# Performance work log

Measured on AMD Instinct MI355X. Metric: run time of the kernel, lower is better.

Reference implementation:

```python
import jax, jax.numpy as jnp
from jax import lax
import numpy as np

B, PEP, MHC, V, H, C, K, NH, FLAT = 1024, 15, 44, 21, 9, 3200, 9, 800, 21 * 59
EPS = 1e-5


def setup_inputs() -> dict:
    key = jax.random.key(0)
    ks = jax.random.split(key, 24)
    n = lambda k, s: jax.random.normal(k, s, dtype=jnp.float32) * 0.05
    inp = {
        'pep': jax.random.normal(ks[0], (B, PEP, V), dtype=jnp.float32),
        'mhc': jax.random.normal(ks[1], (B, MHC, V), dtype=jnp.float32),
        # conv module (bias=True inside CapHLA_EL)
        'W1': n(ks[2], (2 * C, V)), 'b1': n(ks[3], (2 * C,)),
        'Wd': n(ks[4], (C, 1, K)), 'bd': n(ks[5], (C,)),
        'bn1_g': jnp.ones((C,), jnp.float32), 'bn1_b': jnp.zeros((C,), jnp.float32),
        'bn1_m': jnp.zeros((C,), jnp.float32), 'bn1_v': jnp.ones((C,), jnp.float32),
        'W2': n(ks[6], (V, C)), 'b2': n(ks[7], (V,)),
        # shared LayerNorm(vocab_size)
        'ln_g': jnp.ones((V,), jnp.float32), 'ln_b': jnp.zeros((V,), jnp.float32),
        # MHA (bias=False)
        'Wq': n(ks[8], (V, V * H)), 'Wk': n(ks[9], (V, V * H)),
        'Wv': n(ks[10], (V, V * H)), 'Wo': n(ks[11], (V * H, V)),
        # feature selection head
        'Wf1': n(ks[12], (FLAT, NH)), 'bf1': n(ks[13], (NH,)),
        'bn2_g': jnp.ones((NH,), jnp.float32), 'bn2_b': jnp.zeros((NH,), jnp.float32),
        'bn2_m': jnp.zeros((NH,), jnp.float32), 'bn2_v': jnp.ones((NH,), jnp.float32),
        'Wf2': n(ks[14], (NH, 64)), 'bf2': n(ks[15], (64,)),
        'Wf3': n(ks[16], (64, 2)), 'bf3': n(ks[17], (2,)),
    }
    return inp


def _ln(x, g, b):
    m = x.mean(-1, keepdims=True)
    v = x.var(-1, keepdims=True)
    return (x - m) * lax.rsqrt(v + EPS) * g + b


def _forward(pep, mhc, W1, b1, Wd, bd, bn1_g, bn1_b, bn1_m, bn1_v, W2, b2,
             ln_g, ln_b, Wq, Wk, Wv, Wo,
             Wf1, bf1, bn2_g, bn2_b, bn2_m, bn2_v, Wf2, bf2, Wf3, bf3):
    X = jnp.concatenate([pep, mhc], axis=1)  # [B, 59, V]
    residual = X
    # ---- convolution module (channels-first) ----
    x = X.transpose(0, 2, 1)                               # [B, V, L]
    x = jnp.einsum('bcl,oc->bol', x, W1) + b1[None, :, None]   # [B, 2C, L]
    a, g = jnp.split(x, 2, axis=1)
    x = a * jax.nn.sigmoid(g)                              # GLU -> [B, C, L]
    x = lax.conv_general_dilated(x, Wd, window_strides=(1,), padding=[((K - 1) // 2, (K - 1) // 2)],
                                 dimension_numbers=('NCH', 'OIH', 'NCH'),
                                 feature_group_count=C) + bd[None, :, None]
    x = (x - bn1_m[None, :, None]) * lax.rsqrt(bn1_v + EPS)[None, :, None] * bn1_g[None, :, None] + bn1_b[None, :, None]
    x = jax.nn.silu(x)
    x = jnp.einsum('bcl,oc->bol', x, W2) + b2[None, :, None]  # [B, V, L]
    X = _ln(residual + x.transpose(0, 2, 1), ln_g, ln_b)
    residual = X
    # ---- multi-head self-attention (head_dim == V) ----
    Bn, S, D = X.shape
    def heads(W):
        return (X @ W).reshape(Bn, S, H, D).transpose(0, 2, 1, 3)  # [B, H, S, D]
    q, k, v = heads(Wq), heads(Wk), heads(Wv)
    scores = jnp.einsum('bhqd,bhkd->bhqk', q, k) / jnp.sqrt(jnp.float32(D))
    attn = jax.nn.softmax(scores, axis=-1)
    o = jnp.einsum('bhqk,bhkd->bhqd', attn, v)
    o = o.transpose(0, 2, 1, 3).reshape(Bn, S, H * D) @ Wo
    X = _ln(residual + o, ln_g, ln_b)
    # ---- feature selection head ----
    h = X.reshape(Bn, -1) @ Wf1 + bf1
    h = jax.nn.silu(h)
    h = (h - bn2_m) * lax.rsqrt(bn2_v + EPS) * bn2_g + bn2_b
    h = jax.nn.relu(h @ Wf2 + bf2)
    return h @ Wf3 + bf3                                   # [B, 2]


def reference(pep, mhc, W1, b1, Wd, bd, bn1_g, bn1_b, bn1_m, bn1_v, W2, b2,
              ln_g, ln_b, Wq, Wk, Wv, Wo,
              Wf1, bf1, bn2_g, bn2_b, bn2_m, bn2_v, Wf2, bf2, Wf3, bf3):
    return _forward(pep, mhc, W1, b1, Wd, bd, bn1_g, bn1_b, bn1_m, bn1_v, W2, b2,
                    ln_g, ln_b, Wq, Wk, Wv, Wo,
                    Wf1, bf1, bn2_g, bn2_b, bn2_m, bn2_v, Wf2, bf2, Wf3, bf3)
```

## Files before the change

kernel.cpp:

```cpp
#include <hip/hip_runtime.h>
#include <hip/hip_bf16.h>

namespace {

constexpr int B   = 1024;
constexpr int PEP = 15;
constexpr int MHCN = 44;
constexpr int S   = 59;
constexpr int V   = 21;
constexpr int C   = 3200;
constexpr int KW  = 9;
constexpr int H   = 9;
constexpr int NH  = 800;
constexpr int SV  = S * V;
constexpr int HD  = H * V;
constexpr int XF  = 1248;
constexpr float EPSF = 1e-5f;
constexpr int CHALF = 25;
constexpr float NLOG2E = -1.4426950408889634f;

typedef __attribute__((ext_vector_type(8))) short short8;
typedef __attribute__((ext_vector_type(4))) float f32x4;
typedef __attribute__((ext_vector_type(2))) float f32x2;

__device__ __forceinline__ float sigm(float x) {
  return __builtin_amdgcn_rcpf(1.f + __expf(-x));
}
__device__ __forceinline__ unsigned short f2bf(float f) {
  unsigned r;
  asm("v_cvt_pk_bf16_f32 %0, %1, %2" : "=v"(r) : "v"(f), "v"(f));
  return (unsigned short)r;
}
__device__ __forceinline__ unsigned pkbf(float a, float b) {
  unsigned r;
  asm("v_cvt_pk_bf16_f32 %0, %1, %2" : "=v"(r) : "v"(a), "v"(b));
  return r;
}
__device__ __forceinline__ float bflo(unsigned d) {
  union { unsigned u; float f; } v; v.u = d << 16; return v.f;
}
__device__ __forceinline__ float bfhi(unsigned d) {
  union { unsigned u; float f; } v; v.u = d & 0xffff0000u; return v.f;
}

__global__ void k_packW(const float* __restrict__ W1, const float* __restrict__ b1,
                        const float* __restrict__ Wd,
                        const float* __restrict__ bd, const float* __restrict__ g,
                        const float* __restrict__ bb, const float* __restrict__ m,
                        const float* __restrict__ vv, const float* __restrict__ W2,
                        const float* __restrict__ Wq, const float* __restrict__ Wk,
                        const float* __restrict__ Wv, const float* __restrict__ Wo,
                        const float* __restrict__ Wf1,
                        unsigned short* __restrict__ FB1, unsigned short* __restrict__ FB2,
                        unsigned short* __restrict__ FQKV, unsigned short* __restrict__ FWo,
                        unsigned short* __restrict__ FWf1, float* __restrict__ TAP) {
  int id = blockIdx.x * 256 + threadIdx.x;
  if (id < 400 * 64) {
    int tau = id >> 6, l = id & 63;
    int ci = tau >> 3, tt = tau & 7;
    int lr = l & 15, lg = l >> 4;
    bool isg = (tt >= 4);
    int row = (!isg) ? (ci * 64 + tt * 16 + lr) : (C + ci * 64 + (tt - 4) * 16 + lr);
    float sc = isg ? NLOG2E : 1.f;
    for (int j = 0; j < 8; ++j) {
      int k = lg * 8 + j;
      float val = (k < V) ? W1[row * V + k] * sc : (k == V ? b1[row] * sc : 0.f);
      FB1[(size_t)tau * 512 + l * 8 + j] = f2bf(val);
    }
  } else if (id < 38400) {
    int id2 = id - 25600;
    int sg = id2 >> 6, l = id2 & 63;
    int ci = sg >> 2, rem = sg & 3, kt = rem >> 1, nt = rem & 1;
    int lr = l & 15, lg = l >> 4;
    int vc = nt * 16 + lr;
    for (int j = 0; j < 8; ++j) {
      int ch = ci * 64 + kt * 32 + lg * 8 + j;
      float val = (vc < V) ? W2[(size_t)vc * C + ch] : 0.f;
      FB2[(size_t)sg * 512 + l * 8 + j] = f2bf(val);
    }
  } else if (id < 41856) {
    int id2 = id - 38400;
    int tile = id2 >> 6, l = id2 & 63;
    int h = tile / 6, rem = tile - h * 6;
    int mat = rem >> 1, nt = rem & 1;
    int lr = l & 15, kg = l >> 4;
    int dcol = nt * 16 + lr;
    const float* W = (mat == 0) ? Wq : (mat == 1) ? Wk : Wv;
    const float scale = (mat == 0) ? 0.21821789023599236f : 1.f;
    for (int j = 0; j < 8; ++j) {
      int u = kg * 8 + j;
      float val = (u < V && dcol < V) ? W[u * HD + h * V + dcol] * scale : 0.f;
      FQKV[(size_t)tile * 512 + l * 8 + j] = f2bf(val);
    }
  } else if (id < 43008) {
    int id2 = id - 41856;
    int tile = id2 >> 6, l = id2 & 63;
    int h = tile >> 1, nt = tile & 1;
    int lr = l & 15, kg = l >> 4;
    int vcol = nt * 16 + lr;
    for (int j = 0; j < 8; ++j) {
      int d = kg * 8 + j;
      float val = (d < V && vcol < V) ? Wo[(h * V + d) * V + vcol] : 0.f;
      FWo[(size_t)tile * 512 + l * 8 + j] = f2bf(val);
    }
  } else if (id < 46208) {
    int c = id - 43008;
    if (c < C) {
      float sc = g[c] * rsqrtf(vv[c] + EPSF);
      for (int k = 0; k < KW; ++k) TAP[c * 12 + k] = Wd[c * KW + k] * sc;
      TAP[c * 12 + 9]  = (bd[c] - m[c]) * sc + bb[c];
      TAP[c * 12 + 10] = 0.f;
      TAP[c * 12 + 11] = 0.f;
    }
  } else if (id < 46208 + 1950 * 64) {
    int id2 = id - 46208;
    int tile = id2 >> 6, l = id2 & 63;
    int ntg = tile / 39, kk = tile - ntg * 39;
    int lr = l & 15, kg = l >> 4;
    int n = ntg * 16 + lr;
    for (int j = 0; j < 8; ++j) {
      int f = kk * 32 + kg * 8 + j;
      float val = (f < SV) ? Wf1[(size_t)f * NH + n] : 0.f;
      FWf1[(size_t)tile * 512 + l * 8 + j] = f2bf(val);
    }
  }
}

constexpr int GST = 74;

__device__ __forceinline__ void glu_chunk(const unsigned short* fb1p, unsigned* glw0,
                                          short8 ax, int mt, int mypos) {
  f32x4 ga[4], gg[4];
#pragma unroll
  for (int tt = 0; tt < 4; ++tt) {
    short8 bf = *reinterpret_cast<const short8*>(fb1p + tt * 512);
    ga[tt] = __builtin_amdgcn_mfma_f32_16x16x32_bf16(ax, bf, (f32x4){0.f, 0.f, 0.f, 0.f}, 0, 0, 0);
  }
#pragma unroll
  for (int tt = 0; tt < 4; ++tt) {
    short8 bf = *reinterpret_cast<const short8*>(fb1p + (4 + tt) * 512);
    gg[tt] = __builtin_amdgcn_mfma_f32_16x16x32_bf16(ax, bf, (f32x4){0.f, 0.f, 0.f, 0.f}, 0, 0, 0);
  }
  if (mt < 3) {
#pragma unroll
    for (int tt = 0; tt < 4; ++tt) {
      unsigned* gw = glw0 + tt * (16 * GST / 2);
      float s0 = __builtin_amdgcn_rcpf(1.f + __builtin_amdgcn_exp2f(gg[tt][0]));
      float s1 = __builtin_amdgcn_rcpf(1.f + __builtin_amdgcn_exp2f(gg[tt][1]));
      float s2 = __builtin_amdgcn_rcpf(1.f + __builtin_amdgcn_exp2f(gg[tt][2]));
      float s3 = __builtin_amdgcn_rcpf(1.f + __builtin_amdgcn_exp2f(gg[tt][3]));
      gw[0] = pkbf(ga[tt][0] * s0, ga[tt][1] * s1);
      gw[1] = pkbf(ga[tt][2] * s2, ga[tt][3] * s3);
    }
  } else {
#pragma unroll
    for (int tt = 0; tt < 4; ++tt) {
      unsigned* gw = glw0 + tt * (16 * GST / 2);
      float g0 = (mypos + 0 < S) ? ga[tt][0] * __builtin_amdgcn_rcpf(1.f + __builtin_amdgcn_exp2f(gg[tt][0])) : 0.f;
      float g1 = (mypos + 1 < S) ? ga[tt][1] * __builtin_amdgcn_rcpf(1.f + __builtin_amdgcn_exp2f(gg[tt][1])) : 0.f;
      float g2 = (mypos + 2 < S) ? ga[tt][2] * __builtin_amdgcn_rcpf(1.f + __builtin_amdgcn_exp2f(gg[tt][2])) : 0.f;
      float g3 = (mypos + 3 < S) ? ga[tt][3] * __builtin_amdgcn_rcpf(1.f + __builtin_amdgcn_exp2f(gg[tt][3])) : 0.f;
      gw[0] = pkbf(g0, g1);
      gw[1] = pkbf(g2, g3);
    }
  }
}

__device__ __forceinline__ void conv_chunk(const unsigned* glr, const float* tapp,
                                           const unsigned short* fb2p,
                                           unsigned short* sbw, const unsigned short* sbr,
                                           int mt, f32x4 (&acc2)[2]) {
  const float4 t0 = *reinterpret_cast<const float4*>(tapp);
  const float4 t1 = *reinterpret_cast<const float4*>(tapp + 4);
  const float4 t2 = *reinterpret_cast<const float4*>(tapp + 8);
  const float tap[9] = {t0.x, t0.y, t0.z, t0.w, t1.x, t1.y, t1.z, t1.w, t2.x};
  const float sh = t2.y;
  float gv[24];
#pragma unroll
  for (int i2 = 0; i2 < 12; ++i2) {
    const unsigned d = glr[i2];
    gv[2 * i2]     = bflo(d);
    gv[2 * i2 + 1] = bfhi(d);
  }
  f32x2 q[16];
#pragma unroll
  for (int j = 0; j < 16; ++j) q[j] = (f32x2){gv[j], gv[j + 8]};
#pragma unroll
  for (int i2 = 0; i2 < 8; ++i2) {
    f32x2 ac = (f32x2){sh, sh};
#pragma unroll
    for (int k = 0; k < KW; ++k) {
      f32x2 tk = (f32x2){tap[k], tap[k]};
      ac = ac + q[i2 + k] * tk;
    }
    const float a0 = ac.x, a1 = ac.y;
    const float s0 = a0 * __builtin_amdgcn_rcpf(1.f + __builtin_amdgcn_exp2f(a0 * NLOG2E));
    const float s1 = a1 * __builtin_amdgcn_rcpf(1.f + __builtin_amdgcn_exp2f(a1 * NLOG2E));
    sbw[i2 * 72] = f2bf(s0);
    unsigned short hv = f2bf(s1);
    if (mt == 3 && i2 >= 3) hv = 0;
    sbw[(i2 + 8) * 72] = hv;
  }
#pragma unroll
  for (int kt = 0; kt < 2; ++kt) {
    short8 a2f = *reinterpret_cast<const short8*>(sbr + kt * 32);
#pragma unroll
    for (int nt = 0; nt < 2; ++nt) {
      short8 b2f = *reinterpret_cast<const short8*>(fb2p + (kt * 2 + nt) * 512);
      acc2[nt] = __builtin_amdgcn_mfma_f32_16x16x32_bf16(a2f, b2f, acc2[nt], 0, 0, 0);
    }
  }
}

__global__ __launch_bounds__(512) void k_conv(
    const float* __restrict__ pep, const float* __restrict__ mhc,
    const unsigned short* __restrict__ FB1, const unsigned short* __restrict__ FB2,
    const float* __restrict__ TAP, float* __restrict__ Yp) {
  __shared__ __align__(16) unsigned char smem[2 * 64 * GST * 2 + 4 * 16 * 72 * 2];
  unsigned short* Xbf = reinterpret_cast<unsigned short*>(smem);
  unsigned short* glA = reinterpret_cast<unsigned short*>(smem);
  unsigned short* glB = glA + 64 * GST;
  unsigned short* Sb  = glB + 64 * GST;
  const int t = threadIdx.x;
  const int b = blockIdx.x >> 1;
  const int half = blockIdx.x & 1;
  const int lane = t & 63;
  const int w = t >> 6;
  const int lr = lane & 15;
  const int lg = lane >> 4;
  const bool isGlu = (w < 4);
  const int mt = isGlu ? w : (w - 4);
  const int mypos = mt * 16 + lg * 4;

  if (t < 256) {
    const int row = t >> 2, q = t & 3;
    const float* xr = (row < PEP) ? pep + ((size_t)b * PEP + row) * V
                    : (row < S)   ? mhc + ((size_t)b * MHCN + (row - PEP)) * V
                                  : nullptr;
#pragma unroll
    for (int i2 = 0; i2 < 5; ++i2) {
      int c0 = q * 10 + 2 * i2;
      float f0 = (xr && c0 < V) ? xr[c0] : 0.f;
      float f1 = (xr && c0 + 1 < V) ? xr[c0 + 1] : ((xr && c0 + 1 == V) ? 1.f : 0.f);
      *reinterpret_cast<unsigned*>(&Xbf[row * 40 + c0]) = pkbf(f0, f1);
    }
  }
  __syncthreads();

  short8 ax = {};
  if (isGlu) ax = *reinterpret_cast<const short8*>(&Xbf[(mt * 16 + lr) * 40 + lg * 8]);
  __syncthreads();

  if (t < 256) {
    unsigned short* buf = (t < 128) ? glA : glB;
    const int i2 = t & 127;
    *reinterpret_cast<unsigned*>(&buf[(i2 >> 1) * GST + (i2 & 1) * 2]) = 0u;
  }

  f32x4 acc2[2];
  acc2[0] = (f32x4){0.f, 0.f, 0.f, 0.f};
  acc2[1] = (f32x4){0.f, 0.f, 0.f, 0.f};

  unsigned* glwA = reinterpret_cast<unsigned*>(&glA[lr * GST + 4 + mypos]);
  unsigned* glwB = reinterpret_cast<unsigned*>(&glB[lr * GST + 4 + mypos]);
  const unsigned* glrA = reinterpret_cast<const unsigned*>(&glA[lane * GST + mt * 16]);
  const unsigned* glrB = reinterpret_cast<const unsigned*>(&glB[lane * GST + mt * 16]);
  unsigned short* sbw = Sb + mt * (16 * 72) + lane;
  const unsigned short* sbr = Sb + mt * (16 * 72) + lr * 72 + lg * 8;
  const unsigned short* fb1p = FB1 + (size_t)half * CHALF * 8 * 512 + lane * 8;
  const unsigned short* fb2p = FB2 + (size_t)half * CHALF * 4 * 512 + lane * 8;
  const float* tapp = TAP + ((size_t)half * CHALF * 64 + lane) * 12;

  if (isGlu) glu_chunk(fb1p, glwA, ax, mt, mypos);
  __syncthreads();

  for (int p = 0; p < 12; ++p) {
    if (isGlu) glu_chunk(fb1p + 4096, glwB, ax, mt, mypos);
    else       conv_chunk(glrA, tapp, fb2p, sbw, sbr, mt, acc2);
    __syncthreads();
    if (isGlu) glu_chunk(fb1p + 2 * 4096, glwA, ax, mt, mypos);
    else       conv_chunk(glrB, tapp + 768, fb2p + 2048, sbw, sbr, mt, acc2);
    __syncthreads();
    fb1p += 2 * 4096;
    fb2p += 2 * 2048;
    tapp += 2 * 768;
  }
  if (!isGlu) {
    conv_chunk(glrA, tapp, fb2p, sbw, sbr, mt, acc2);
    float* yp = Yp + (size_t)blockIdx.x * SV;
#pragma unroll
    for (int nt = 0; nt < 2; ++nt) {
#pragma unroll
      for (int r = 0; r < 4; ++r) {
        const int pos = mypos + r, vc = nt * 16 + lr;
        if (pos < S && vc < V) yp[pos * V + vc] = acc2[nt][r];
      }
    }
  }
}

__global__ __launch_bounds__(64) void k_ln(
    const float* __restrict__ pep, const float* __restrict__ mhc,
    const float* __restrict__ Yp, const float* __restrict__ b2,
    const float* __restrict__ lng, const float* __restrict__ lnb,
    float* __restrict__ X1) {
  const int t = threadIdx.x;
  const int b = blockIdx.x;
  if (t >= S) return;
  const float* xr = (t < PEP) ? pep + ((size_t)b * PEP + t) * V
                              : mhc + ((size_t)b * MHCN + (t - PEP)) * V;
  const float* y0 = Yp + (size_t)(2 * b) * SV + t * V;
  const float* y1 = y0 + SV;
  float z[V];
  float mn = 0.f;
#pragma unroll
  for (int v = 0; v < V; ++v) {
    z[v] = xr[v] + (y0[v] + y1[v]) + b2[v];
    mn += z[v];
  }
  mn *= (1.f / V);
  float var = 0.f;
#pragma unroll
  for (int v = 0; v < V; ++v) {
    float d = z[v] - mn;
    var = fmaf(d, d, var);
  }
  const float inv = rsqrtf(var * (1.f / V) + EPSF);
#pragma unroll
  for (int v = 0; v < V; ++v)
    X1[(size_t)b * SV + t * V + v] = (z[v] - mn) * inv * lng[v] + lnb[v];
}

__global__ __launch_bounds__(256) void k_attn(
    const float* __restrict__ X1, const unsigned short* __restrict__ FQKV,
    const unsigned short* __restrict__ FWo, const float* __restrict__ lng,
    const float* __restrict__ lnb, unsigned short* __restrict__ X2bf) {
  __shared__ float X1f[64 * 21];
  __shared__ __align__(16) unsigned short Qb[64 * 40];
  __shared__ __align__(16) unsigned short Kb[64 * 40];
  __shared__ __align__(16) unsigned short Vt[32 * 72];
  __shared__ __align__(16) unsigned short Pt[64 * 72];
  __shared__ __align__(16) unsigned short Oh[64 * 40];
  const int t = threadIdx.x;
  const int b = blockIdx.x;
  const int lane = t & 63;
  const int w = t >> 6;
  const int lr = lane & 15;
  const int lg = lane >> 4;
  const int mypos = w * 16 + lg * 4;

  for (int i = t; i < 64 * 21; i += 256)
    X1f[i] = (i < SV) ? X1[(size_t)b * SV + i] : 0.f;
  __syncthreads();

  short8 ax;
  {
    const int rowi = w * 16 + lr;
#pragma unroll
    for (int j = 0; j < 8; ++j) {
      int col = lg * 8 + j;
      ax[j] = (short)((col < V) ? f2bf(X1f[rowi * 21 + col]) : (unsigned short)0);
    }
  }
  f32x4 accw[2];
  accw[0] = (f32x4){0.f, 0.f, 0.f, 0.f};
  accw[1] = (f32x4){0.f, 0.f, 0.f, 0.f};

  for (int h = 0; h < H; ++h) {
    const unsigned short* fq = FQKV + (size_t)(h * 6) * 512;
    f32x4 dq[2], dk[2], dv[2];
#pragma unroll
    for (int nt = 0; nt < 2; ++nt) {
      short8 bq = *reinterpret_cast<const short8*>(fq + (0 + nt) * 512 + lane * 8);
      dq[nt] = __builtin_amdgcn_mfma_f32_16x16x32_bf16(ax, bq, (f32x4){0.f, 0.f, 0.f, 0.f}, 0, 0, 0);
      short8 bk = *reinterpret_cast<const short8*>(fq + (2 + nt) * 512 + lane * 8);
      dk[nt] = __builtin_amdgcn_mfma_f32_16x16x32_bf16(ax, bk, (f32x4){0.f, 0.f, 0.f, 0.f}, 0, 0, 0);
      short8 bv = *reinterpret_cast<const short8*>(fq + (4 + nt) * 512 + lane * 8);
      dv[nt] = __builtin_amdgcn_mfma_f32_16x16x32_bf16(ax, bv, (f32x4){0.f, 0.f, 0.f, 0.f}, 0, 0, 0);
    }
#pragma unroll
    for (int nt = 0; nt < 2; ++nt) {
      const int d = nt * 16 + lr;
#pragma unroll
      for (int r = 0; r < 4; ++r) {
        const int pos = mypos + r;
        Qb[pos * 40 + d] = f2bf(dq[nt][r]);
        Kb[pos * 40 + d] = f2bf(dk[nt][r]);
      }
      *reinterpret_cast<unsigned*>(&Vt[d * 72 + mypos])     = pkbf(dv[nt][0], dv[nt][1]);
      *reinterpret_cast<unsigned*>(&Vt[d * 72 + mypos + 2]) = pkbf(dv[nt][2], dv[nt][3]);
    }
    __syncthreads();

    short8 bqf = *reinterpret_cast<const short8*>(&Qb[(w * 16 + lr) * 40 + lg * 8]);
    f32x4 st[4];
#pragma unroll
    for (int mt = 0; mt < 4; ++mt) {
      short8 akf = *reinterpret_cast<const short8*>(&Kb[(mt * 16 + lr) * 40 + lg * 8]);
      st[mt] = __builtin_amdgcn_mfma_f32_16x16x32_bf16(akf, bqf, (f32x4){0.f, 0.f, 0.f, 0.f}, 0, 0, 0);
    }
    float mx = -1e30f;
#pragma unroll
    for (int mt = 0; mt < 4; ++mt)
#pragma unroll
      for (int r = 0; r < 4; ++r) {
        const int j = mt * 16 + lg * 4 + r;
        float sv = (j < S) ? st[mt][r] : -1e30f;
        st[mt][r] = sv;
        mx = fmaxf(mx, sv);
      }
    mx = fmaxf(mx, __shfl_xor(mx, 16));
    mx = fmaxf(mx, __shfl_xor(mx, 32));
    float sum = 0.f;
#pragma unroll
    for (int mt = 0; mt < 4; ++mt)
#pragma unroll
      for (int r = 0; r < 4; ++r) {
        float e = __expf(st[mt][r] - mx);
        st[mt][r] = e;
        sum += e;
      }
    sum += __shfl_xor(sum, 16);
    sum += __shfl_xor(sum, 32);
#pragma unroll
    for (int mt = 0; mt < 4; ++mt) {
#pragma unroll
      for (int s2 = 0; s2 < 2; ++s2) {
        *reinterpret_cast<unsigned*>(&Pt[(w * 16 + lr) * 72 + mt * 16 + lg * 4 + 2 * s2]) =
            pkbf(st[mt][2 * s2], st[mt][2 * s2 + 1]);
      }
    }
    short8 bp0 = *reinterpret_cast<const short8*>(&Pt[(w * 16 + lr) * 72 + lg * 8]);
    short8 bp1 = *reinterpret_cast<const short8*>(&Pt[(w * 16 + lr) * 72 + 32 + lg * 8]);
    f32x4 ot[2];
    ot[0] = (f32x4){0.f, 0.f, 0.f, 0.f};
    ot[1] = (f32x4){0.f, 0.f, 0.f, 0.f};
#pragma unroll
    for (int mt = 0; mt < 2; ++mt) {
      short8 av0 = *reinterpret_cast<const short8*>(&Vt[(mt * 16 + lr) * 72 + lg * 8]);
      ot[mt] = __builtin_amdgcn_mfma_f32_16x16x32_bf16(av0, bp0, ot[mt], 0, 0, 0);
      short8 av1 = *reinterpret_cast<const short8*>(&Vt[(mt * 16 + lr) * 72 + 32 + lg * 8]);
      ot[mt] = __builtin_amdgcn_mfma_f32_16x16x32_bf16(av1, bp1, ot[mt], 0, 0, 0);
    }
    const float inv = __builtin_amdgcn_rcpf(sum);
#pragma unroll
    for (int mt = 0; mt < 2; ++mt) {
#pragma unroll
      for (int s2 = 0; s2 < 2; ++s2) {
        *reinterpret_cast<unsigned*>(&Oh[(w * 16 + lr) * 40 + mt * 16 + lg * 4 + 2 * s2]) =
            pkbf(ot[mt][2 * s2] * inv, ot[mt][2 * s2 + 1] * inv);
      }
    }
    short8 ao = *reinterpret_cast<const short8*>(&Oh[(w * 16 + lr) * 40 + lg * 8]);
#pragma unroll
    for (int nt = 0; nt < 2; ++nt) {
      short8 bw = *reinterpret_cast<const short8*>(FWo + (size_t)(h * 2 + nt) * 512 + lane * 8);
      accw[nt] = __builtin_amdgcn_mfma_f32_16x16x32_bf16(ao, bw, accw[nt], 0, 0, 0);
    }
    __syncthreads();
  }

#pragma unroll
  for (int r = 0; r < 4; ++r) {
    const int pos = mypos + r;
    const bool v1ok = (lr < 5);
    const float x0 = (pos < S) ? X1f[pos * 21 + lr] : 0.f;
    const float x1 = (v1ok && pos < S) ? X1f[pos * 21 + 16 + lr] : 0.f;
    float z0 = accw[0][r] + x0;
    float z1 = v1ok ? (accw[1][r] + x1) : 0.f;
    float s = z0 + z1;
    s += __shfl_xor(s, 1); s += __shfl_xor(s, 2);
    s += __shfl_xor(s, 4); s += __shfl_xor(s, 8);
    const float mn = s * (1.f / V);
    const float d0 = z0 - mn;
    const float d1 = v1ok ? (z1 - mn) : 0.f;
    float vq = d0 * d0 + d1 * d1;
    vq += __shfl_xor(vq, 1); vq += __shfl_xor(vq, 2);
    vq += __shfl_xor(vq, 4); vq += __shfl_xor(vq, 8);
    const float inv = rsqrtf(vq * (1.f / V) + EPSF);
    if (pos < S) {
      X2bf[(size_t)b * XF + pos * 21 + lr] = f2bf(d0 * inv * lng[lr] + lnb[lr]);
      if (v1ok)
        X2bf[(size_t)b * XF + pos * 21 + 16 + lr] = f2bf(d1 * inv * lng[16 + lr] + lnb[16 + lr]);
    }
  }
  if (t < XF - SV) X2bf[(size_t)b * XF + SV + t] = 0;
}

__global__ __launch_bounds__(256) void k_f1(
    const unsigned short* __restrict__ X2bf, const unsigned short* __restrict__ FWf1,
    const float* __restrict__ bf1, const float* __restrict__ g2,
    const float* __restrict__ bb2, const float* __restrict__ m2,
    const float* __restrict__ v2, float* __restrict__ Hb) {
  const int t = threadIdx.x;
  const int lane = t & 63;
  const int w = t >> 6;
  const int lr = lane & 15;
  const int lg = lane >> 4;
  const int Mb = blockIdx.x * 64;
  const int NbT = blockIdx.y * 5;

  const unsigned short* ap = X2bf + (size_t)(Mb + w * 16 + lr) * XF + lg * 8;
  const unsigned short* bp = FWf1 + (size_t)NbT * 39 * 512 + lane * 8;
  f32x4 acc[5];
#pragma unroll
  for (int nt = 0; nt < 5; ++nt) acc[nt] = (f32x4){0.f, 0.f, 0.f, 0.f};

  for (int kk = 0; kk < 39; ++kk) {
    short8 af = *reinterpret_cast<const short8*>(ap + kk * 32);
#pragma unroll
    for (int nt = 0; nt < 5; ++nt) {
      short8 bf = *reinterpret_cast<const short8*>(bp + ((size_t)nt * 39 + kk) * 512);
      acc[nt] = __builtin_amdgcn_mfma_f32_16x16x32_bf16(af, bf, acc[nt], 0, 0, 0);
    }
  }
#pragma unroll
  for (int nt = 0; nt < 5; ++nt) {
    const int n = (NbT + nt) * 16 + lr;
    const float sc = g2[n] * rsqrtf(v2[n] + EPSF);
    const float sh = bb2[n] - m2[n] * sc;
    const float bias = bf1[n];
#pragma unroll
    for (int r = 0; r < 4; ++r) {
      const int row = Mb + w * 16 + lg * 4 + r;
      float hh = acc[nt][r] + bias;
      hh = fmaf(hh * sigm(hh), sc, sh);
      Hb[(size_t)row * NH + n] = hh;
    }
  }
}

__global__ __launch_bounds__(64) void k_f23(
    const float* __restrict__ Hb, const float* __restrict__ Wf2, const float* __restrict__ bf2,
    const float* __restrict__ Wf3, const float* __restrict__ bf3, float* __restrict__ out) {
  __shared__ __align__(16) float hs[NH];
  const int t = threadIdx.x;
  const int b = blockIdx.x;
  for (int i = t; i < NH; i += 64) hs[i] = Hb[(size_t)b * NH + i];
  __syncthreads();
  float acc = bf2[t];
  for (int n = 0; n < NH; n += 4) {
    const float4 hv = *reinterpret_cast<const float4*>(&hs[n]);
    acc = fmaf(hv.x, Wf2[n * 64 + t], acc);
    acc = fmaf(hv.y, Wf2[(n + 1) * 64 + t], acc);
    acc = fmaf(hv.z, Wf2[(n + 2) * 64 + t], acc);
    acc = fmaf(hv.w, Wf2[(n + 3) * 64 + t], acc);
  }
  const float mid = fmaxf(acc, 0.f);
  float p0 = mid * Wf3[t * 2 + 0];
  float p1 = mid * Wf3[t * 2 + 1];
#pragma unroll
  for (int off = 32; off > 0; off >>= 1) {
    p0 += __shfl_down(p0, off);
    p1 += __shfl_down(p1, off);
  }
  if (t == 0) {
    out[b * 2 + 0] = p0 + bf3[0];
    out[b * 2 + 1] = p1 + bf3[1];
  }
}

}

extern "C" void kernel_launch(void* const* d_in, const int* in_sizes, int n_in,
                              void* d_out, int out_size, void* d_ws, size_t ws_size,
                              hipStream_t stream) {
  const float* pep   = (const float*)d_in[0];
  const float* mhc   = (const float*)d_in[1];
  const float* W1    = (const float*)d_in[2];
  const float* b1    = (const float*)d_in[3];
  const float* Wd    = (const float*)d_in[4];
  const float* bd    = (const float*)d_in[5];
  const float* bn1_g = (const float*)d_in[6];
  const float* bn1_b = (const float*)d_in[7];
  const float* bn1_m = (const float*)d_in[8];
  const float* bn1_v = (const float*)d_in[9];
  const float* W2    = (const float*)d_in[10];
  const float* b2    = (const float*)d_in[11];
  const float* ln_g  = (const float*)d_in[12];
  const float* ln_b  = (const float*)d_in[13];
  const float* Wq    = (const float*)d_in[14];
  const float* Wk    = (const float*)d_in[15];
  const float* Wv    = (const float*)d_in[16];
  const float* Wo    = (const float*)d_in[17];
  const float* Wf1   = (const float*)d_in[18];
  const float* bf1   = (const float*)d_in[19];
  const float* bn2_g = (const float*)d_in[20];
  const float* bn2_b = (const float*)d_in[21];
  const float* bn2_m = (const float*)d_in[22];
  const float* bn2_v = (const float*)d_in[23];
  const float* Wf2   = (const float*)d_in[24];
  const float* bf2   = (const float*)d_in[25];
  const float* Wf3   = (const float*)d_in[26];
  const float* bf3   = (const float*)d_in[27];
  float* out = (float*)d_out;

  float* ws = (float*)d_ws;
  float* X1 = ws;
  unsigned short* X2bf = (unsigned short*)(X1 + (size_t)B * SV);
  float* Hb = (float*)(X2bf + (size_t)B * XF);
  float* TAP = Hb + (size_t)B * NH;
  unsigned short* FB1  = (unsigned short*)(TAP + (size_t)C * 12);
  unsigned short* FB2  = FB1 + (size_t)400 * 512;
  unsigned short* FQKV = FB2 + (size_t)200 * 512;
  unsigned short* FWo  = FQKV + (size_t)54 * 512;
  unsigned short* FWf1 = FWo + (size_t)18 * 512;
  float* Yp = (float*)(FWf1 + (size_t)1950 * 512);

  k_packW<<<669, 256, 0, stream>>>(W1, b1, Wd, bd, bn1_g, bn1_b, bn1_m, bn1_v, W2,
                                   Wq, Wk, Wv, Wo, Wf1, FB1, FB2, FQKV, FWo, FWf1, TAP);
  k_conv<<<2 * B, 512, 0, stream>>>(pep, mhc, FB1, FB2, TAP, Yp);
  k_ln<<<B, 64, 0, stream>>>(pep, mhc, Yp, b2, ln_g, ln_b, X1);
  k_attn<<<B, 256, 0, stream>>>(X1, FQKV, FWo, ln_g, ln_b, X2bf);
  dim3 g5(16, 10);
  k_f1<<<g5, 256, 0, stream>>>(X2bf, FWf1, bf1, bn2_g, bn2_b, bn2_m, bn2_v, Hb);
  k_f23<<<B, 64, 0, stream>>>(Hb, Wf2, bf2, Wf3, bf3, out);
}
```

Before: 245.5 us.

## Split conv channels into quarters per batch and fuse LayerNorm into attention

The conv kernel now splits the channel range across four blocks per batch element (13/13/13/11 chunks) instead of two, doubling the grid to raise parallelism and shorten the per-block serial chunk loop. The separate LayerNorm kernel is removed. Its residual-add, four-way partial-sum reduction and normalisation now run inside the attention kernel's shared-memory load, which drops one launch and the X1 round trip through global memory. The trade-off is redundant per-block input staging and twice as many partial outputs written to and read from Yp.

Result: slower. 256.0 us (+4.3%).

```diff
diff --git a/kernel.cpp b/kernel.cpp
--- a/kernel.cpp
+++ b/kernel.cpp
@@ -16,7 +16,6 @@
 constexpr int HD  = H * V;
 constexpr int XF  = 1248;
 constexpr float EPSF = 1e-5f;
-constexpr int CHALF = 25;
 constexpr float NLOG2E = -1.4426950408889634f;
 
 typedef __attribute__((ext_vector_type(8))) short short8;
@@ -127,6 +126,8 @@
 }
 
 constexpr int GST = 74;
+__constant__ const int QOFF[4] = {0, 13, 26, 39};
+__constant__ const int QNP[4]  = {6, 6, 6, 5};
 
 __device__ __forceinline__ void glu_chunk(const unsigned short* fb1p, unsigned* glw0,
                                           short8 ax, int mt, int mypos) {
@@ -222,8 +223,8 @@
   unsigned short* glB = glA + 64 * GST;
   unsigned short* Sb  = glB + 64 * GST;
   const int t = threadIdx.x;
-  const int b = blockIdx.x >> 1;
-  const int half = blockIdx.x & 1;
+  const int b = blockIdx.x >> 2;
+  const int q = blockIdx.x & 3;
   const int lane = t & 63;
   const int w = t >> 6;
   const int lr = lane & 15;
@@ -231,15 +232,17 @@
   const bool isGlu = (w < 4);
   const int mt = isGlu ? w : (w - 4);
   const int mypos = mt * 16 + lg * 4;
+  const int qoff = QOFF[q];
+  const int npairs = QNP[q];
 
   if (t < 256) {
-    const int row = t >> 2, q = t & 3;
+    const int row = t >> 2, qq = t & 3;
     const float* xr = (row < PEP) ? pep + ((size_t)b * PEP + row) * V
                     : (row < S)   ? mhc + ((size_t)b * MHCN + (row - PEP)) * V
                                   : nullptr;
 #pragma unroll
     for (int i2 = 0; i2 < 5; ++i2) {
-      int c0 = q * 10 + 2 * i2;
+      int c0 = qq * 10 + 2 * i2;
       float f0 = (xr && c0 < V) ? xr[c0] : 0.f;
       float f1 = (xr && c0 + 1 < V) ? xr[c0 + 1] : ((xr && c0 + 1 == V) ? 1.f : 0.f);
       *reinterpret_cast<unsigned*>(&Xbf[row * 40 + c0]) = pkbf(f0, f1);
@@ -267,14 +270,14 @@
   const unsigned* glrB = reinterpret_cast<const unsigned*>(&glB[lane * GST + mt * 16]);
   unsigned short* sbw = Sb + mt * (16 * 72) + lane;
   const unsigned short* sbr = Sb + mt * (16 * 72) + lr * 72 + lg * 8;
-  const unsigned short* fb1p = FB1 + (size_t)half * CHALF * 8 * 512 + lane * 8;
-  const unsigned short* fb2p = FB2 + (size_t)half * CHALF * 4 * 512 + lane * 8;
-  const float* tapp = TAP + ((size_t)half * CHALF * 64 + lane) * 12;
+  const unsigned short* fb1p = FB1 + (size_t)qoff * 8 * 512 + lane * 8;
+  const unsigned short* fb2p = FB2 + (size_t)qoff * 4 * 512 + lane * 8;
+  const float* tapp = TAP + ((size_t)qoff * 64 + lane) * 12;
 
   if (isGlu) glu_chunk(fb1p, glwA, ax, mt, mypos);
   __syncthreads();
 
-  for (int p = 0; p < 12; ++p) {
+  for (int p = 0; p < npairs; ++p) {
     if (isGlu) glu_chunk(fb1p + 4096, glwB, ax, mt, mypos);
     else       conv_chunk(glrA, tapp, fb2p, sbw, sbr, mt, acc2);
     __syncthreads();
@@ -299,40 +302,10 @@
   }
 }
 
-__global__ __launch_bounds__(64) void k_ln(
+__global__ __launch_bounds__(256) void k_attn(
     const float* __restrict__ pep, const float* __restrict__ mhc,
     const float* __restrict__ Yp, const float* __restrict__ b2,
-    const float* __restrict__ lng, const float* __restrict__ lnb,
-    float* __restrict__ X1) {
-  const int t = threadIdx.x;
-  const int b = blockIdx.x;
-  if (t >= S) return;
-  const float* xr = (t < PEP) ? pep + ((size_t)b * PEP + t) * V
-                              : mhc + ((size_t)b * MHCN + (t - PEP)) * V;
-  const float* y0 = Yp + (size_t)(2 * b) * SV + t * V;
-  const float* y1 = y0 + SV;
-  float z[V];
-  float mn = 0.f;
-#pragma unroll
-  for (int v = 0; v < V; ++v) {
-    z[v] = xr[v] + (y0[v] + y1[v]) + b2[v];
-    mn += z[v];
-  }
-  mn *= (1.f / V);
-  float var = 0.f;
-#pragma unroll
-  for (int v = 0; v < V; ++v) {
-    float d = z[v] - mn;
-    var = fmaf(d, d, var);
-  }
-  const float inv = rsqrtf(var * (1.f / V) + EPSF);
-#pragma unroll
-  for (int v = 0; v < V; ++v)
-    X1[(size_t)b * SV + t * V + v] = (z[v] - mn) * inv * lng[v] + lnb[v];
-}
-
-__global__ __launch_bounds__(256) void k_attn(
-    const float* __restrict__ X1, const unsigned short* __restrict__ FQKV,
+    const unsigned short* __restrict__ FQKV,
     const unsigned short* __restrict__ FWo, const float* __restrict__ lng,
     const float* __restrict__ lnb, unsigned short* __restrict__ X2bf) {
   __shared__ float X1f[64 * 21];
@@ -349,8 +322,34 @@
   const int lg = lane >> 4;
   const int mypos = w * 16 + lg * 4;
 
-  for (int i = t; i < 64 * 21; i += 256)
-    X1f[i] = (i < SV) ? X1[(size_t)b * SV + i] : 0.f;
+  if (t < 64) {
+    if (t < S) {
+      const float* xr = (t < PEP) ? pep + ((size_t)b * PEP + t) * V
+                                  : mhc + ((size_t)b * MHCN + (t - PEP)) * V;
+      const float* y0 = Yp + (size_t)(4 * b) * SV + t * V;
+      float z[V];
+      float mn = 0.f;
+#pragma unroll
+      for (int v = 0; v < V; ++v) {
+        z[v] = xr[v] + ((y0[v] + y0[SV + v]) + (y0[2 * SV + v] + y0[3 * SV + v])) + b2[v];
+        mn += z[v];
+      }
+      mn *= (1.f / V);
+      float var = 0.f;
+#pragma unroll
+      for (int v = 0; v < V; ++v) {
+        float d = z[v] - mn;
+        var = fmaf(d, d, var);
+      }
+      const float inv = rsqrtf(var * (1.f / V) + EPSF);
+#pragma unroll
+      for (int v = 0; v < V; ++v)
+        X1f[t * 21 + v] = (z[v] - mn) * inv * lng[v] + lnb[v];
+    } else {
+#pragma unroll
+      for (int v = 0; v < V; ++v) X1f[t * 21 + v] = 0.f;
+    }
+  }
   __syncthreads();
 
   short8 ax;
@@ -596,8 +595,7 @@
   float* out = (float*)d_out;
 
   float* ws = (float*)d_ws;
-  float* X1 = ws;
-  unsigned short* X2bf = (unsigned short*)(X1 + (size_t)B * SV);
+  unsigned short* X2bf = (unsigned short*)ws;
   float* Hb = (float*)(X2bf + (size_t)B * XF);
   float* TAP = Hb + (size_t)B * NH;
   unsigned short* FB1  = (unsigned short*)(TAP + (size_t)C * 12);
@@ -609,9 +607,8 @@
 
   k_packW<<<669, 256, 0, stream>>>(W1, b1, Wd, bd, bn1_g, bn1_b, bn1_m, bn1_v, W2,
                                    Wq, Wk, Wv, Wo, Wf1, FB1, FB2, FQKV, FWo, FWf1, TAP);
-  k_conv<<<2 * B, 512, 0, stream>>>(pep, mhc, FB1, FB2, TAP, Yp);
-  k_ln<<<B, 64, 0, stream>>>(pep, mhc, Yp, b2, ln_g, ln_b, X1);
-  k_attn<<<B, 256, 0, stream>>>(X1, FQKV, FWo, ln_g, ln_b, X2bf);
+  k_conv<<<4 * B, 512, 0, stream>>>(pep, mhc, FB1, FB2, TAP, Yp);
+  k_attn<<<B, 256, 0, stream>>>(pep, mhc, Yp, b2, FQKV, FWo, ln_g, ln_b, X2bf);
   dim3 g5(16, 10);
   k_f1<<<g5, 256, 0, stream>>>(X2bf, FWf1, bf1, bn2_g, bn2_b, bn2_m, bn2_v, Hb);
   k_f23<<<B, 64, 0, stream>>>(Hb, Wf2, bf2, Wf3, bf3, out);
```
